# Kernel optimization log

Measured on AMD Instinct MI355X. Metric: run time of the kernel, lower is better.

Reference implementation:

```python
import jax, jax.numpy as jnp
import numpy as np

S, B, G, P = 8, 8192, 512, 16
E, H, BOT = 64, 64, 1024

def setup_inputs() -> dict:
    key = jax.random.key(0)
    k = jax.random.split(key, 9)
    in_xy = jax.random.normal(k[0], (S, B, 2), dtype=jnp.float32)
    in_dxdy = jax.random.normal(k[1], (S, B, 2), dtype=jnp.float32)
    h_states = jax.random.normal(k[2], (1, B, H), dtype=jnp.float32)
    starts = jnp.arange(G, dtype=jnp.int64) * P
    seq_start_end = jnp.stack([starts, starts + P], axis=1)
    W_emb = jax.random.normal(k[3], (2, E), dtype=jnp.float32) / jnp.sqrt(2.0)
    b_emb = jnp.zeros((E,), dtype=jnp.float32)
    W1 = jax.random.normal(k[4], (E + H, H), dtype=jnp.float32) / jnp.sqrt(float(E + H))
    b1 = jnp.zeros((H,), dtype=jnp.float32)
    W2 = jax.random.normal(k[5], (H, BOT), dtype=jnp.float32) / jnp.sqrt(float(H))
    b2 = jnp.zeros((BOT,), dtype=jnp.float32)
    return {"in_xy": in_xy, "in_dxdy": in_dxdy, "h_states": h_states,
            "seq_start_end": seq_start_end, "W_emb": W_emb, "b_emb": b_emb,
            "W1": W1, "b1": b1, "W2": W2, "b2": b2}

def reference(in_xy, in_dxdy, h_states, seq_start_end, W_emb, b_emb, W1, b1, W2, b2):
    # Uniform group size: P = batch / num_groups (groups are contiguous).
    batch = in_xy.shape[1]
    g = seq_start_end.shape[0]
    p = batch // g
    end_pos = in_xy[-1].reshape(g, p, 2)            # (G,P,2)
    h = h_states.reshape(batch, -1).reshape(g, p, -1)  # (G,P,H)
    # torch semantics: row (i*P+j) of the pair matrix uses pos[j]-pos[i], hidden[j]
    rel = end_pos[:, None, :, :] - end_pos[:, :, None, :]  # (G,P_i,P_j,2)
    emb = rel @ W_emb + b_emb                              # (G,P,P,E)
    hj = jnp.broadcast_to(h[:, None, :, :], (g, p, p, h.shape[-1]))
    x = jnp.concatenate([emb, hj], axis=-1)                # (G,P,P,E+H)
    x = jax.nn.relu(x @ W1 + b1)
    x = jax.nn.relu(x @ W2 + b2)                           # (G,P,P,BOT)
    pool = jnp.max(x, axis=2)                              # max over j -> (G,P,BOT)
    return pool.reshape(batch, -1)
```

## Files before the change

### kernel.cpp

```cpp
#include <hip/hip_runtime.h>
#include <hip/hip_bf16.h>

typedef __attribute__((ext_vector_type(8))) short bf16x8;
typedef __attribute__((ext_vector_type(4))) float f32x4;

#define NB 8192
#define NS 8

__device__ __forceinline__ unsigned short f2bf(float f) {
  union { float f; unsigned int u; } v; v.f = f;
  unsigned int r = v.u + 0x7FFFu + ((v.u >> 16) & 1u);
  return (unsigned short)(r >> 16);
}

__global__ __launch_bounds__(256) void prep_kernel(
    const float* __restrict__ W2, const float* __restrict__ W_emb,
    const float* __restrict__ b_emb, const float* __restrict__ W1,
    unsigned short* __restrict__ w2f, float* __restrict__ wc,
    unsigned short* __restrict__ w1bf) {
  int tid = blockIdx.x * 256 + threadIdx.x;
  if (tid < 8192) {
    int lane = tid & 63;
    int ks = (tid >> 6) & 1;
    int nt = tid >> 7;
    int col = nt * 16 + (lane & 15);
    int k0 = ks * 32 + (lane >> 4) * 8;
    bf16x8 pk;
#pragma unroll
    for (int e = 0; e < 8; ++e)
      pk[e] = (short)f2bf(W2[(k0 + e) * 1024 + col]);
    *(bf16x8*)(w2f + tid * 8) = pk;
  } else if (tid < 8192 + 192) {
    int t2 = tid - 8192;
    int c = t2 >> 6, k = t2 & 63;
    float s = 0.f;
    for (int e = 0; e < 64; ++e) {
      float src = (c < 2) ? W_emb[c * 64 + e] : b_emb[e];
      s += src * W1[e * 64 + k];
    }
    wc[t2] = s;
  } else if (tid < 8192 + 192 + 512) {
    int q = tid - 8384;
    int lane = q & 63;
    int fr = q >> 6;
    int nt = fr >> 1, ks = fr & 1;
    int col = nt * 16 + (lane & 15);
    int e0 = ks * 32 + (lane >> 4) * 8;
    bf16x8 pk;
#pragma unroll
    for (int e = 0; e < 8; ++e)
      pk[e] = (short)f2bf(W1[(64 + e0 + e) * 64 + col]);
    *(bf16x8*)(w1bf + q * 8) = pk;
  }
}

__global__ __launch_bounds__(256, 4) void pool_kernel(
    const float* __restrict__ in_xy, const float* __restrict__ h_states,
    const float* __restrict__ b1, const float* __restrict__ b2,
    const unsigned short* __restrict__ w2f, const float* __restrict__ wc,
    const unsigned short* __restrict__ w1bf, float* __restrict__ out) {
  __shared__ bf16x8 Afrag[2048];
  __shared__ float hWs[16][72];
  __shared__ float exy[32];
  const int g = blockIdx.x >> 1;
  const int half = blockIdx.x & 1;
  const int t = threadIdx.x;
  const int lane = t & 63;
  const int wv = t >> 6;

  if (t < 32) {
    int p = t & 15;
    exy[t] = in_xy[((NS - 1) * NB + g * 16 + p) * 2 + (t >> 4)];
  }

  {
    const int row = g * 16 + (lane & 15);
    const int e0 = (lane >> 4) * 8;
    const float* hp = h_states + row * 64 + e0;
    bf16x8 ha0, ha1;
#pragma unroll
    for (int e = 0; e < 8; ++e) {
      ha0[e] = (short)f2bf(hp[e]);
      ha1[e] = (short)f2bf(hp[e + 32]);
    }
    bf16x8 bf0 = *(const bf16x8*)(w1bf + ((wv * 2 + 0) * 64 + lane) * 8);
    bf16x8 bf1 = *(const bf16x8*)(w1bf + ((wv * 2 + 1) * 64 + lane) * 8);
    f32x4 z = {0.f, 0.f, 0.f, 0.f};
    f32x4 acc = __builtin_amdgcn_mfma_f32_16x16x32_bf16(ha0, bf0, z, 0, 0, 0);
    acc = __builtin_amdgcn_mfma_f32_16x16x32_bf16(ha1, bf1, acc, 0, 0, 0);
    int col = wv * 16 + (lane & 15);
    float bb = b1[col] + wc[128 + col];
#pragma unroll
    for (int r = 0; r < 4; ++r)
      hWs[(lane >> 4) * 4 + r][col] = acc[r] + bb;
  }

  float b2v[8];
#pragma unroll
  for (int u = 0; u < 8; ++u)
    b2v[u] = b2[half * 512 + wv * 128 + u * 16 + (lane & 15)];
  const int i = t & 15;
  const int k0 = ((t >> 6) & 1) * 32 + ((t >> 4) & 3) * 8;
  float w0[8], w1[8];
#pragma unroll
  for (int e = 0; e < 8; ++e) {
    w0[e] = wc[k0 + e];
    w1[e] = wc[64 + k0 + e];
  }
  __syncthreads();

  {
    float exi = exy[i], eyi = exy[16 + i];
#pragma unroll
    for (int c = 0; c < 8; ++c) {
      int j = (t >> 7) + 2 * c;
      float rx = exy[j] - exi;
      float ry = exy[16 + j] - eyi;
      const f32x4* hp2 = (const f32x4*)&hWs[j][k0];
      f32x4 h0 = hp2[0], h1 = hp2[1];
      float hv[8] = {h0[0], h0[1], h0[2], h0[3], h1[0], h1[1], h1[2], h1[3]};
      bf16x8 pk;
#pragma unroll
      for (int e = 0; e < 8; ++e) {
        float v = fmaf(rx, w0[e], fmaf(ry, w1[e], hv[e]));
        v = fmaxf(v, 0.f);
        pk[e] = (short)f2bf(v);
      }
      Afrag[t + 256 * c] = pk;
    }
  }
  __syncthreads();

  const int rowbase = (g * 16 + (lane >> 4) * 4) * 1024 + half * 512 + wv * 128 + (lane & 15);
  const bf16x8* ap = Afrag + lane;
  const f32x4 NEGINF = {-3.4e38f, -3.4e38f, -3.4e38f, -3.4e38f};
#pragma unroll
  for (int pass = 0; pass < 2; ++pass) {
    bf16x8 bfr[4][2];
#pragma unroll
    for (int u = 0; u < 4; ++u) {
      int nt = half * 32 + wv * 8 + pass * 4 + u;
      bfr[u][0] = *(const bf16x8*)(w2f + ((nt * 2 + 0) * 64 + lane) * 8);
      bfr[u][1] = *(const bf16x8*)(w2f + ((nt * 2 + 1) * 64 + lane) * 8);
    }
    f32x4 pool[4], accB[4];
#pragma unroll
    for (int u = 0; u < 4; ++u) { pool[u] = NEGINF; accB[u] = NEGINF; }

    bf16x8 a0 = ap[0];
    bf16x8 a1 = ap[64];
#pragma unroll
    for (int jj = 0; jj < 16; jj += 2) {
      f32x4 accA[4];
      __builtin_amdgcn_s_setprio(1);
#pragma unroll
      for (int u = 0; u < 4; ++u) {
        f32x4 z = {0.f, 0.f, 0.f, 0.f};
        accA[u] = __builtin_amdgcn_mfma_f32_16x16x32_bf16(a0, bfr[u][0], z, 0, 0, 0);
      }
#pragma unroll
      for (int u = 0; u < 4; ++u)
        accA[u] = __builtin_amdgcn_mfma_f32_16x16x32_bf16(a1, bfr[u][1], accA[u], 0, 0, 0);
      __builtin_amdgcn_s_setprio(0);
      bf16x8 c0 = ap[(jj + 1) * 128];
      bf16x8 c1 = ap[(jj + 1) * 128 + 64];
#pragma unroll
      for (int u = 0; u < 4; ++u)
#pragma unroll
        for (int r = 0; r < 4; ++r) pool[u][r] = fmaxf(pool[u][r], accB[u][r]);

      __builtin_amdgcn_s_setprio(1);
#pragma unroll
      for (int u = 0; u < 4; ++u) {
        f32x4 z = {0.f, 0.f, 0.f, 0.f};
        accB[u] = __builtin_amdgcn_mfma_f32_16x16x32_bf16(c0, bfr[u][0], z, 0, 0, 0);
      }
#pragma unroll
      for (int u = 0; u < 4; ++u)
        accB[u] = __builtin_amdgcn_mfma_f32_16x16x32_bf16(c1, bfr[u][1], accB[u], 0, 0, 0);
      __builtin_amdgcn_s_setprio(0);
      int jn = (jj + 2) & 15;
      a0 = ap[jn * 128];
      a1 = ap[jn * 128 + 64];
#pragma unroll
      for (int u = 0; u < 4; ++u)
#pragma unroll
        for (int r = 0; r < 4; ++r) pool[u][r] = fmaxf(pool[u][r], accA[u][r]);
    }
#pragma unroll
    for (int u = 0; u < 4; ++u)
#pragma unroll
      for (int r = 0; r < 4; ++r) pool[u][r] = fmaxf(pool[u][r], accB[u][r]);

#pragma unroll
    for (int u = 0; u < 4; ++u) {
      float bb = b2v[pass * 4 + u];
#pragma unroll
      for (int r = 0; r < 4; ++r)
        out[rowbase + r * 1024 + (pass * 4 + u) * 16] = fmaxf(pool[u][r] + bb, 0.f);
    }
  }
}

extern "C" void kernel_launch(void* const* d_in, const int* in_sizes, int n_in,
                              void* d_out, int out_size, void* d_ws, size_t ws_size,
                              hipStream_t stream) {
  const float* in_xy = (const float*)d_in[0];
  const float* h_states = (const float*)d_in[2];
  const float* W_emb = (const float*)d_in[4];
  const float* b_emb = (const float*)d_in[5];
  const float* W1 = (const float*)d_in[6];
  const float* b1 = (const float*)d_in[7];
  const float* W2 = (const float*)d_in[8];
  const float* b2 = (const float*)d_in[9];
  float* out = (float*)d_out;

  unsigned short* w2f = (unsigned short*)d_ws;
  float* wc = (float*)((char*)d_ws + 131072);
  unsigned short* w1bf = (unsigned short*)((char*)d_ws + 132096);

  prep_kernel<<<35, 256, 0, stream>>>(W2, W_emb, b_emb, W1, w2f, wc, w1bf);
  pool_kernel<<<1024, 256, 0, stream>>>(in_xy, h_states, b1, b2, w2f, wc, w1bf, out);
}
```

Baseline: 28.23 us.

## Fuse weight preparation into pool kernel and drop the separate prep launch

After: 34.26 us. 1.21x slower.

```diff
diff --git a/kernel.cpp b/kernel.cpp
--- a/kernel.cpp
+++ b/kernel.cpp
@@ -13,54 +13,15 @@
   return (unsigned short)(r >> 16);
 }
 
-__global__ __launch_bounds__(256) void prep_kernel(
-    const float* __restrict__ W2, const float* __restrict__ W_emb,
-    const float* __restrict__ b_emb, const float* __restrict__ W1,
-    unsigned short* __restrict__ w2f, float* __restrict__ wc,
-    unsigned short* __restrict__ w1bf) {
-  int tid = blockIdx.x * 256 + threadIdx.x;
-  if (tid < 8192) {
-    int lane = tid & 63;
-    int ks = (tid >> 6) & 1;
-    int nt = tid >> 7;
-    int col = nt * 16 + (lane & 15);
-    int k0 = ks * 32 + (lane >> 4) * 8;
-    bf16x8 pk;
-#pragma unroll
-    for (int e = 0; e < 8; ++e)
-      pk[e] = (short)f2bf(W2[(k0 + e) * 1024 + col]);
-    *(bf16x8*)(w2f + tid * 8) = pk;
-  } else if (tid < 8192 + 192) {
-    int t2 = tid - 8192;
-    int c = t2 >> 6, k = t2 & 63;
-    float s = 0.f;
-    for (int e = 0; e < 64; ++e) {
-      float src = (c < 2) ? W_emb[c * 64 + e] : b_emb[e];
-      s += src * W1[e * 64 + k];
-    }
-    wc[t2] = s;
-  } else if (tid < 8192 + 192 + 512) {
-    int q = tid - 8384;
-    int lane = q & 63;
-    int fr = q >> 6;
-    int nt = fr >> 1, ks = fr & 1;
-    int col = nt * 16 + (lane & 15);
-    int e0 = ks * 32 + (lane >> 4) * 8;
-    bf16x8 pk;
-#pragma unroll
-    for (int e = 0; e < 8; ++e)
-      pk[e] = (short)f2bf(W1[(64 + e0 + e) * 64 + col]);
-    *(bf16x8*)(w1bf + q * 8) = pk;
-  }
-}
-
 __global__ __launch_bounds__(256, 4) void pool_kernel(
     const float* __restrict__ in_xy, const float* __restrict__ h_states,
-    const float* __restrict__ b1, const float* __restrict__ b2,
-    const unsigned short* __restrict__ w2f, const float* __restrict__ wc,
-    const unsigned short* __restrict__ w1bf, float* __restrict__ out) {
+    const float* __restrict__ W_emb, const float* __restrict__ b_emb,
+    const float* __restrict__ W1, const float* __restrict__ b1,
+    const float* __restrict__ W2, const float* __restrict__ b2,
+    float* __restrict__ out) {
   __shared__ bf16x8 Afrag[2048];
   __shared__ float hWs[16][72];
+  __shared__ float wcs[192];
   __shared__ float exy[32];
   const int g = blockIdx.x >> 1;
   const int half = blockIdx.x & 1;
@@ -72,27 +33,36 @@
     int p = t & 15;
     exy[t] = in_xy[((NS - 1) * NB + g * 16 + p) * 2 + (t >> 4)];
   }
-
+  if (t < 192) {
+    int c = t >> 6, k = t & 63;
+    const float* src = (c == 0) ? W_emb : (c == 1) ? (W_emb + 64) : b_emb;
+    float s0 = 0.f, s1 = 0.f;
+    for (int e = 0; e < 64; e += 2) {
+      s0 = fmaf(src[e], W1[e * 64 + k], s0);
+      s1 = fmaf(src[e + 1], W1[(e + 1) * 64 + k], s1);
+    }
+    wcs[t] = s0 + s1;
+  }
   {
     const int row = g * 16 + (lane & 15);
     const int e0 = (lane >> 4) * 8;
     const float* hp = h_states + row * 64 + e0;
-    bf16x8 ha0, ha1;
+    const float* wp = W1 + (64 + e0) * 64 + wv * 16 + (lane & 15);
+    bf16x8 ha0, ha1, bf0, bf1;
 #pragma unroll
     for (int e = 0; e < 8; ++e) {
       ha0[e] = (short)f2bf(hp[e]);
       ha1[e] = (short)f2bf(hp[e + 32]);
+      bf0[e] = (short)f2bf(wp[e * 64]);
+      bf1[e] = (short)f2bf(wp[(e + 32) * 64]);
     }
-    bf16x8 bf0 = *(const bf16x8*)(w1bf + ((wv * 2 + 0) * 64 + lane) * 8);
-    bf16x8 bf1 = *(const bf16x8*)(w1bf + ((wv * 2 + 1) * 64 + lane) * 8);
     f32x4 z = {0.f, 0.f, 0.f, 0.f};
     f32x4 acc = __builtin_amdgcn_mfma_f32_16x16x32_bf16(ha0, bf0, z, 0, 0, 0);
     acc = __builtin_amdgcn_mfma_f32_16x16x32_bf16(ha1, bf1, acc, 0, 0, 0);
     int col = wv * 16 + (lane & 15);
-    float bb = b1[col] + wc[128 + col];
 #pragma unroll
     for (int r = 0; r < 4; ++r)
-      hWs[(lane >> 4) * 4 + r][col] = acc[r] + bb;
+      hWs[(lane >> 4) * 4 + r][col] = acc[r];
   }
 
   float b2v[8];
@@ -101,15 +71,16 @@
     b2v[u] = b2[half * 512 + wv * 128 + u * 16 + (lane & 15)];
   const int i = t & 15;
   const int k0 = ((t >> 6) & 1) * 32 + ((t >> 4) & 3) * 8;
-  float w0[8], w1[8];
-#pragma unroll
-  for (int e = 0; e < 8; ++e) {
-    w0[e] = wc[k0 + e];
-    w1[e] = wc[64 + k0 + e];
-  }
   __syncthreads();
 
   {
+    float w0[8], w1[8], bias8[8];
+#pragma unroll
+    for (int e = 0; e < 8; ++e) {
+      w0[e] = wcs[k0 + e];
+      w1[e] = wcs[64 + k0 + e];
+      bias8[e] = b1[k0 + e] + wcs[128 + k0 + e];
+    }
     float exi = exy[i], eyi = exy[16 + i];
 #pragma unroll
     for (int c = 0; c < 8; ++c) {
@@ -122,7 +93,7 @@
       bf16x8 pk;
 #pragma unroll
       for (int e = 0; e < 8; ++e) {
-        float v = fmaf(rx, w0[e], fmaf(ry, w1[e], hv[e]));
+        float v = fmaf(rx, w0[e], fmaf(ry, w1[e], hv[e] + bias8[e]));
         v = fmaxf(v, 0.f);
         pk[e] = (short)f2bf(v);
       }
@@ -133,6 +104,7 @@
 
   const int rowbase = (g * 16 + (lane >> 4) * 4) * 1024 + half * 512 + wv * 128 + (lane & 15);
   const bf16x8* ap = Afrag + lane;
+  const float* w2p = W2 + ((lane >> 4) * 8) * 1024 + (lane & 15);
   const f32x4 NEGINF = {-3.4e38f, -3.4e38f, -3.4e38f, -3.4e38f};
 #pragma unroll
   for (int pass = 0; pass < 2; ++pass) {
@@ -140,8 +112,12 @@
 #pragma unroll
     for (int u = 0; u < 4; ++u) {
       int nt = half * 32 + wv * 8 + pass * 4 + u;
-      bfr[u][0] = *(const bf16x8*)(w2f + ((nt * 2 + 0) * 64 + lane) * 8);
-      bfr[u][1] = *(const bf16x8*)(w2f + ((nt * 2 + 1) * 64 + lane) * 8);
+      const float* p0 = w2p + nt * 16;
+#pragma unroll
+      for (int e = 0; e < 8; ++e) {
+        bfr[u][0][e] = (short)f2bf(p0[e * 1024]);
+        bfr[u][1][e] = (short)f2bf(p0[(e + 32) * 1024]);
+      }
     }
     f32x4 pool[4], accB[4];
 #pragma unroll
@@ -196,8 +172,10 @@
     for (int u = 0; u < 4; ++u) {
       float bb = b2v[pass * 4 + u];
 #pragma unroll
-      for (int r = 0; r < 4; ++r)
-        out[rowbase + r * 1024 + (pass * 4 + u) * 16] = fmaxf(pool[u][r] + bb, 0.f);
+      for (int r = 0; r < 4; ++r) {
+        float res = fmaxf(pool[u][r] + bb, 0.f);
+        __builtin_nontemporal_store(res, &out[rowbase + r * 1024 + (pass * 4 + u) * 16]);
+      }
     }
   }
 }
@@ -215,10 +193,6 @@
   const float* b2 = (const float*)d_in[9];
   float* out = (float*)d_out;
 
-  unsigned short* w2f = (unsigned short*)d_ws;
-  float* wc = (float*)((char*)d_ws + 131072);
-  unsigned short* w1bf = (unsigned short*)((char*)d_ws + 132096);
-
-  prep_kernel<<<35, 256, 0, stream>>>(W2, W_emb, b_emb, W1, w2f, wc, w1bf);
-  pool_kernel<<<1024, 256, 0, stream>>>(in_xy, h_states, b1, b2, w2f, wc, w1bf, out);
+  pool_kernel<<<1024, 256, 0, stream>>>(in_xy, h_states, W_emb, b_emb, W1, b1,
+                                        W2, b2, out);
 }
```
